# Performance work log

Hardware: AMD Instinct MI355X
Metric: run time of the kernel (lower is better)

Reference implementation:

```python
import jax, jax.numpy as jnp
import numpy as np

K = 3          # k_neighbors
EPS = 1e-12    # F.normalize eps


def _l2norm(x):
    n = jnp.sqrt(jnp.sum(x * x, axis=-1, keepdims=True))
    return x / jnp.maximum(n, EPS)


def setup_inputs() -> dict:
    key = jax.random.key(0)
    k1, k2 = jax.random.split(key)
    query_features = jax.random.normal(k1, (64, 64, 32, 32), dtype=jnp.float32)
    support_features = jax.random.normal(k2, (64, 5, 64, 1024), dtype=jnp.float32)
    return {"query_features": query_features, "support_features": support_features}


def reference(query_features, support_features):
    B, D, h, w = query_features.shape
    # (B, Nq, D), L2-normalized along D
    q_local = _l2norm(query_features.reshape(B, D, h * w).transpose(0, 2, 1))
    # support: (B, Way, D, Ns) -> (B, Way, Ns, D), L2-normalized along D
    s_local = _l2norm(support_features.transpose(0, 1, 3, 2))
    # cosine similarities for all (batch, way) pairs in one batched matmul
    sim = jnp.einsum('bqd,bwsd->bwqs', q_local, s_local)  # (B, Way, Nq, Ns)
    k_actual = min(K, sim.shape[-1])
    topk_sim, _ = jax.lax.top_k(sim, k_actual)            # (B, Way, Nq, k)
    return topk_sim.sum(axis=(-1, -2))                    # (B, Way)
```

## Files before the change

### kernel.cpp

```cpp
#include <hip/hip_runtime.h>
#include <hip/hip_bf16.h>


using bf16x8 = __attribute__((ext_vector_type(8))) short;
using f32x4  = __attribute__((ext_vector_type(4))) float;

__device__ inline unsigned cvt_pk_bf16(float lo, float hi) {
    unsigned r;
    asm("v_cvt_pk_bf16_f32 %0, %1, %2" : "=v"(r) : "v"(lo), "v"(hi));
    return r;
}

__device__ inline uint4 pack8cvt(const float* v) {
    uint4 r;
    r.x = cvt_pk_bf16(v[0], v[1]);
    r.y = cvt_pk_bf16(v[2], v[3]);
    r.z = cvt_pk_bf16(v[4], v[5]);
    r.w = cvt_pk_bf16(v[6], v[7]);
    return r;
}

#define INS(v, T0, T1, T2) do {                         \
    float _v = (v);                                     \
    float _n0 = fmaxf((T0), _v);                        \
    float _n1 = __builtin_amdgcn_fmed3f(_v, (T0), (T1));\
    float _n2 = __builtin_amdgcn_fmed3f(_v, (T1), (T2));\
    (T0) = _n0; (T1) = _n1; (T2) = _n2;                 \
} while (0)

__device__ inline void gload16(const void* g, void* lds) {
    __builtin_amdgcn_global_load_lds(
        (const __attribute__((address_space(1))) unsigned int*)g,
        (__attribute__((address_space(3))) unsigned int*)lds,
        16, 0, 0);
}


__global__ __launch_bounds__(256) void prep_all(const float* __restrict__ Q,
                                                const float* __restrict__ S,
                                                uint4* __restrict__ Qbf,
                                                uint4* __restrict__ Sbf,
                                                float* __restrict__ rnq) {
    const int blk = blockIdx.x;
    if (blk < 256) {
        const int b = blk >> 2;
        const int col = ((blk & 3) << 8) + threadIdx.x;
        const float* p = Q + (size_t)b * 65536 + col;
        float v[64];
        #pragma unroll
        for (int d = 0; d < 64; ++d) v[d] = p[(size_t)d << 10];
        float ss = 0.f;
        #pragma unroll
        for (int d = 0; d < 64; ++d) ss += v[d] * v[d];
        rnq[(b << 10) + col] = 1.0f / fmaxf(sqrtf(ss), 1e-12f);
        uint4* ob = Qbf + ((size_t)(b << 6) + (col >> 4)) * 128 + (col & 15);
        #pragma unroll
        for (int h = 0; h < 8; ++h)
            ob[h << 4] = pack8cvt(&v[h << 3]);
    } else {
        const int bw = (blk - 256) >> 2;
        const int col = ((blk & 3) << 8) + threadIdx.x;
        const float* p = S + (size_t)bw * 65536 + col;
        float v[64];
        #pragma unroll
        for (int d = 0; d < 64; ++d) v[d] = p[(size_t)d << 10];
        float ss = 0.f;
        #pragma unroll
        for (int d = 0; d < 64; ++d) ss += v[d] * v[d];
        const float rs = 1.0f / fmaxf(sqrtf(ss), 1e-12f);
        #pragma unroll
        for (int d = 0; d < 64; ++d) v[d] *= rs;
        uint4* ob = Sbf + ((size_t)(bw << 6) + (col >> 4)) * 128 + (col & 15);
        #pragma unroll
        for (int h = 0; h < 8; ++h)
            ob[h << 4] = pack8cvt(&v[h << 3]);
    }
}

__device__ __forceinline__ void compute_tile4(const uint4* sp, int lane,
                                              const bf16x8 (&bq)[4][2],
                                              float (&t0)[4], float (&t1)[4],
                                              float (&t2)[4]) {
    bf16x8 a0 = *reinterpret_cast<const bf16x8*>(&sp[lane]);
    bf16x8 a1 = *reinterpret_cast<const bf16x8*>(&sp[64 + lane]);
    const f32x4 z = {0.f, 0.f, 0.f, 0.f};
    f32x4 c[4];
    __builtin_amdgcn_s_setprio(1);
    #pragma unroll
    for (int qt = 0; qt < 4; ++qt) {
        c[qt] = __builtin_amdgcn_mfma_f32_16x16x32_bf16(a0, bq[qt][0], z, 0, 0, 0);
        c[qt] = __builtin_amdgcn_mfma_f32_16x16x32_bf16(a1, bq[qt][1], c[qt], 0, 0, 0);
    }
    __builtin_amdgcn_s_setprio(0);
    #pragma unroll
    for (int qt = 0; qt < 4; ++qt) {
        INS(c[qt][0], t0[qt], t1[qt], t2[qt]);
        INS(c[qt][1], t0[qt], t1[qt], t2[qt]);
        INS(c[qt][2], t0[qt], t1[qt], t2[qt]);
        INS(c[qt][3], t0[qt], t1[qt], t2[qt]);
    }
}

__global__ __launch_bounds__(256, 4) void knn_main(const uint4* __restrict__ Qbf,
                                                   const uint4* __restrict__ Sbf,
                                                   const float* __restrict__ rnq,
                                                   float* __restrict__ partial) {
    __shared__ uint4 ring[4][5 * 128];
    const int lin = blockIdx.x;
    const int l   = (lin & 7) * 320 + (lin >> 3);
    const int qc  = l & 7;
    const int bw  = l >> 3;
    const int b   = bw / 5;
    const int wv = threadIdx.x >> 6, lane = threadIdx.x & 63;
    const int g  = wv >> 1, h = wv & 1;

    const uint4* qb = Qbf + ((size_t)(b << 6) + (qc << 3) + (g << 2)) * 128 + lane;
    bf16x8 bq[4][2];
    #pragma unroll
    for (int qt = 0; qt < 4; ++qt)
        #pragma unroll
        for (int c = 0; c < 2; ++c)
            bq[qt][c] = *reinterpret_cast<const bf16x8*>(&qb[qt * 128 + (c << 6)]);

    const char* sbyte = (const char*)(Sbf + (size_t)bw * 8192) + ((size_t)h << 16)
                        + (size_t)lane * 16;
    uint4* myring = &ring[wv][0];

    float t0[4], t1[4], t2[4];
    #pragma unroll
    for (int qt = 0; qt < 4; ++qt) { t0[qt] = -1e30f; t1[qt] = -1e30f; t2[qt] = -1e30f; }

    #pragma unroll
    for (int t = 0; t < 3; ++t) {
        gload16(sbyte + (size_t)t * 2048,        &myring[t * 128]);
        gload16(sbyte + (size_t)t * 2048 + 1024, &myring[t * 128 + 64]);
    }

    int rslot = 0, wslot = 3;
    for (int t = 0; t <= 28; ++t) {
        gload16(sbyte + (size_t)(t + 3) * 2048,        &myring[wslot * 128]);
        gload16(sbyte + (size_t)(t + 3) * 2048 + 1024, &myring[wslot * 128 + 64]);
        asm volatile("s_waitcnt vmcnt(6)" ::: "memory");
        compute_tile4(&myring[rslot * 128], lane, bq, t0, t1, t2);
        if (++rslot == 5) rslot = 0;
        if (++wslot == 5) wslot = 0;
    }
    asm volatile("s_waitcnt vmcnt(4)" ::: "memory");
    compute_tile4(&myring[4 * 128], lane, bq, t0, t1, t2);
    asm volatile("s_waitcnt vmcnt(2)" ::: "memory");
    compute_tile4(&myring[0], lane, bq, t0, t1, t2);
    asm volatile("s_waitcnt vmcnt(0)" ::: "memory");
    compute_tile4(&myring[1 * 128], lane, bq, t0, t1, t2);

    #pragma unroll
    for (int qt = 0; qt < 4; ++qt) {
        #pragma unroll
        for (int m = 16; m <= 32; m <<= 1) {
            float b0 = __shfl_xor(t0[qt], m);
            float b1 = __shfl_xor(t1[qt], m);
            float b2 = __shfl_xor(t2[qt], m);
            INS(b0, t0[qt], t1[qt], t2[qt]);
            INS(b1, t0[qt], t1[qt], t2[qt]);
            INS(b2, t0[qt], t1[qt], t2[qt]);
        }
    }

    if (h == 1) {
        float* tb = (float*)&ring[wv][0];
        if (lane < 16) {
            #pragma unroll
            for (int qt = 0; qt < 4; ++qt) {
                tb[qt * 48 + lane]      = t0[qt];
                tb[qt * 48 + 16 + lane] = t1[qt];
                tb[qt * 48 + 32 + lane] = t2[qt];
            }
        }
    }
    __syncthreads();
    if (h == 0) {
        const float* tb = (const float*)&ring[wv + 1][0];
        float s3 = 0.f;
        #pragma unroll
        for (int qt = 0; qt < 4; ++qt) {
            float u0 = tb[qt * 48 + (lane & 15)];
            float u1 = tb[qt * 48 + 16 + (lane & 15)];
            float u2 = tb[qt * 48 + 32 + (lane & 15)];
            INS(u0, t0[qt], t1[qt], t2[qt]);
            INS(u1, t0[qt], t1[qt], t2[qt]);
            INS(u2, t0[qt], t1[qt], t2[qt]);
            const int qg = (qc << 7) + (g << 6) + (qt << 4) + (lane & 15);
            s3 += (t0[qt] + t1[qt] + t2[qt]) * rnq[(b << 10) + qg];
        }
        #pragma unroll
        for (int m = 1; m < 64; m <<= 1) s3 += __shfl_xor(s3, m);
        s3 *= 0.25f;
        if (lane == 0) partial[(size_t)bw * 16 + qc * 2 + g] = s3;
    }
}

__global__ void finalize16(const float* __restrict__ partial, float* __restrict__ out) {
    int i = blockIdx.x * blockDim.x + threadIdx.x;
    if (i < 320) {
        float a = 0.f;
        #pragma unroll
        for (int k = 0; k < 16; ++k) a += partial[16 * i + k];
        out[i] = a;
    }
}

__global__ void norms_kernel(const float* __restrict__ Q, const float* __restrict__ S,
                             float* __restrict__ rnq, float* __restrict__ rns) {
    int gid = blockIdx.x * blockDim.x + threadIdx.x;
    if (gid < 65536) {
        int b = gid >> 10, qi = gid & 1023;
        const float* p = Q + (size_t)b * 65536 + qi;
        float ss = 0.f;
        #pragma unroll
        for (int d = 0; d < 64; ++d) { float v = p[(size_t)d * 1024]; ss += v * v; }
        rnq[gid] = 1.0f / fmaxf(sqrtf(ss), 1e-12f);
    } else {
        int v = gid - 65536;
        int bw = v >> 10, si = v & 1023;
        const float* p = S + (size_t)bw * 65536 + si;
        float ss = 0.f;
        #pragma unroll
        for (int d = 0; d < 64; ++d) { float x = p[(size_t)d * 1024]; ss += x * x; }
        rns[v] = 1.0f / fmaxf(sqrtf(ss), 1e-12f);
    }
}

__global__ __launch_bounds__(512, 4) void knn_fb(
        const float* __restrict__ Q, const float* __restrict__ S,
        const float* __restrict__ rnq, const float* __restrict__ rns,
        float* __restrict__ partial) {
    __shared__ uint4 qfrag[16 * 128];
    __shared__ uint4 sfrag[2][4 * 128];
    __shared__ float wsum[8];

    const int qc = blockIdx.x, w = blockIdx.y, b = blockIdx.z;
    const int t = threadIdx.x, wv = t >> 6, lane = t & 63;

    const float* Qb   = Q + (size_t)b * 65536;
    const float* Sb   = S + (size_t)(b * 5 + w) * 65536;
    const float* rnqb = rnq + (b << 10);
    const float* rnsb = rns + ((b * 5 + w) << 10);

    bf16x8 bq[4][2];
    for (int ph = 0; ph < 2; ++ph) {
        for (int sub = 0; sub < 4; ++sub) {
            int qg = (qc << 9) + (ph << 8) + (sub << 6) + lane;
            float v[8];
            #pragma unroll
            for (int i = 0; i < 8; ++i)
                v[i] = Qb[(size_t)((wv << 3) + i) * 1024 + qg];
            qfrag[((sub << 2) + (lane >> 4)) * 128 + (wv << 4) + (lane & 15)] = pack8cvt(v);
        }
        __syncthreads();
        if ((wv >> 2) == ph) {
            #pragma unroll
            for (int qt = 0; qt < 4; ++qt)
                #pragma unroll
                for (int c = 0; c < 2; ++c)
                    bq[qt][c] = *reinterpret_cast<const bf16x8*>(
                        &qfrag[(((wv & 3) << 2) + qt) * 128 + (c << 6) + lane]);
        }
        __syncthreads();
    }

    {
        float sv[8]; float rs = rnsb[lane];
        #pragma unroll
        for (int i = 0; i < 8; ++i)
            sv[i] = Sb[(size_t)((wv << 3) + i) * 1024 + lane] * rs;
        sfrag[0][(lane >> 4) * 128 + (wv << 4) + (lane & 15)] = pack8cvt(sv);
    }
    __syncthreads();

    float t0[4], t1[4], t2[4];
    #pragma unroll
    for (int qt = 0; qt < 4; ++qt) { t0[qt] = -1e30f; t1[qt] = -1e30f; t2[qt] = -1e30f; }
    int cur = 0;
    const float* sp = Sb + ((wv << 3) << 10) + lane;

    for (int blk = 0; blk < 16; ++blk) {
        float sv[8]; float rs;
        if (blk < 15) {
            const int sb_ = (blk + 1) << 6;
            rs = rnsb[sb_ + lane];
            #pragma unroll
            for (int i = 0; i < 8; ++i)
                sv[i] = sp[(size_t)(i << 10) + sb_];
        }
        #pragma unroll
        for (int st = 0; st < 4; ++st) {
            bf16x8 a0 = *reinterpret_cast<const bf16x8*>(&sfrag[cur][st * 128 + lane]);
            bf16x8 a1 = *reinterpret_cast<const bf16x8*>(&sfrag[cur][st * 128 + 64 + lane]);
            #pragma unroll
            for (int qt = 0; qt < 4; ++qt) {
                f32x4 c = {0.f, 0.f, 0.f, 0.f};
                c = __builtin_amdgcn_mfma_f32_16x16x32_bf16(a0, bq[qt][0], c, 0, 0, 0);
                c = __builtin_amdgcn_mfma_f32_16x16x32_bf16(a1, bq[qt][1], c, 0, 0, 0);
                #pragma unroll
                for (int j = 0; j < 4; ++j)
                    INS(c[j], t0[qt], t1[qt], t2[qt]);
            }
        }
        if (blk < 15) {
            #pragma unroll
            for (int i = 0; i < 8; ++i) sv[i] *= rs;
            sfrag[cur ^ 1][(lane >> 4) * 128 + (wv << 4) + (lane & 15)] = pack8cvt(sv);
        }
        __syncthreads();
        cur ^= 1;
    }

    float s3 = 0.f;
    #pragma unroll
    for (int qt = 0; qt < 4; ++qt) {
        #pragma unroll
        for (int m = 16; m <= 32; m <<= 1) {
            float b0 = __shfl_xor(t0[qt], m);
            float b1 = __shfl_xor(t1[qt], m);
            float b2 = __shfl_xor(t2[qt], m);
            INS(b0, t0[qt], t1[qt], t2[qt]);
            INS(b1, t0[qt], t1[qt], t2[qt]);
            INS(b2, t0[qt], t1[qt], t2[qt]);
        }
        int qg = (qc << 9) + (wv << 6) + (qt << 4) + (lane & 15);
        s3 += (t0[qt] + t1[qt] + t2[qt]) * rnqb[qg];
    }
    #pragma unroll
    for (int m = 1; m < 64; m <<= 1) s3 += __shfl_xor(s3, m);
    s3 *= 0.25f;
    if (lane == 0) wsum[wv] = s3;
    __syncthreads();
    if (t == 0) {
        float acc = 0.f;
        #pragma unroll
        for (int i = 0; i < 8; ++i) acc += wsum[i];
        partial[((b * 5 + w) << 1) + qc] = acc;
    }
}

__global__ void finalize2(const float* __restrict__ partial, float* __restrict__ out) {
    int i = blockIdx.x * blockDim.x + threadIdx.x;
    if (i < 320)
        out[i] = partial[2 * i] + partial[2 * i + 1];
}

extern "C" void kernel_launch(void* const* d_in, const int* in_sizes, int n_in,
                              void* d_out, int out_size, void* d_ws, size_t ws_size,
                              hipStream_t stream) {
    const float* Q = (const float*)d_in[0];
    const float* S = (const float*)d_in[1];
    float* out = (float*)d_out;

    const size_t QBF = 8388608ull, SBF = 41943040ull, RNQ = 262144ull;
    const size_t NEED = QBF + SBF + RNQ + 20480ull;
    if (ws_size >= NEED) {
        char* base = (char*)d_ws;
        uint4* Qbf     = (uint4*)base;
        uint4* Sbf     = (uint4*)(base + QBF);
        float* rnq     = (float*)(base + QBF + SBF);
        float* partial = (float*)(base + QBF + SBF + RNQ);
        prep_all<<<1536, 256, 0, stream>>>(Q, S, Qbf, Sbf, rnq);
        knn_main<<<2560, 256, 0, stream>>>(Qbf, Sbf, rnq, partial);
        finalize16<<<2, 256, 0, stream>>>(partial, out);
    } else {
        float* rnq = (float*)d_ws;
        float* rns = rnq + 65536;
        float* partial = rns + 327680;
        norms_kernel<<<(65536 + 327680) / 256, 256, 0, stream>>>(Q, S, rnq, rns);
        knn_fb<<<dim3(2, 5, 64), 512, 0, stream>>>(Q, S, rnq, rns, partial);
        finalize2<<<2, 256, 0, stream>>>(partial, out);
    }
}
```

Before: 95.42 us.

## Software-pipeline MFMA with top-k insertion and prefetch LDS reads one tile ahead

Restructures the main loop so the MFMAs for tile t overlap the top-3 insertion of tile t-1 and the LDS reads for tile t+1, with the loop fully unrolled. The launch bounds change from min 4 blocks per CU to waves_per_eu(1,2), giving the compiler more registers for the doubled accumulator and operand sets. The aim is to hide MFMA latency and LDS latency behind VALU work. In exchange, occupancy may drop and code size grows, and the vmcnt accounting changes with the staggered loads.

```diff
diff --git a/kernel.cpp b/kernel.cpp
--- a/kernel.cpp
+++ b/kernel.cpp
@@ -77,34 +77,12 @@
     }
 }
 
-__device__ __forceinline__ void compute_tile4(const uint4* sp, int lane,
-                                              const bf16x8 (&bq)[4][2],
-                                              float (&t0)[4], float (&t1)[4],
-                                              float (&t2)[4]) {
-    bf16x8 a0 = *reinterpret_cast<const bf16x8*>(&sp[lane]);
-    bf16x8 a1 = *reinterpret_cast<const bf16x8*>(&sp[64 + lane]);
-    const f32x4 z = {0.f, 0.f, 0.f, 0.f};
-    f32x4 c[4];
-    __builtin_amdgcn_s_setprio(1);
-    #pragma unroll
-    for (int qt = 0; qt < 4; ++qt) {
-        c[qt] = __builtin_amdgcn_mfma_f32_16x16x32_bf16(a0, bq[qt][0], z, 0, 0, 0);
-        c[qt] = __builtin_amdgcn_mfma_f32_16x16x32_bf16(a1, bq[qt][1], c[qt], 0, 0, 0);
-    }
-    __builtin_amdgcn_s_setprio(0);
-    #pragma unroll
-    for (int qt = 0; qt < 4; ++qt) {
-        INS(c[qt][0], t0[qt], t1[qt], t2[qt]);
-        INS(c[qt][1], t0[qt], t1[qt], t2[qt]);
-        INS(c[qt][2], t0[qt], t1[qt], t2[qt]);
-        INS(c[qt][3], t0[qt], t1[qt], t2[qt]);
-    }
-}
-
-__global__ __launch_bounds__(256, 4) void knn_main(const uint4* __restrict__ Qbf,
-                                                   const uint4* __restrict__ Sbf,
-                                                   const float* __restrict__ rnq,
-                                                   float* __restrict__ partial) {
+__global__ __launch_bounds__(256)
+__attribute__((amdgpu_waves_per_eu(1, 2)))
+void knn_main(const uint4* __restrict__ Qbf,
+              const uint4* __restrict__ Sbf,
+              const float* __restrict__ rnq,
+              float* __restrict__ partial) {
     __shared__ uint4 ring[4][5 * 128];
     const int lin = blockIdx.x;
     const int l   = (lin & 7) * 320 + (lin >> 3);
@@ -130,27 +108,60 @@
     #pragma unroll
     for (int qt = 0; qt < 4; ++qt) { t0[qt] = -1e30f; t1[qt] = -1e30f; t2[qt] = -1e30f; }
 
-    #pragma unroll
-    for (int t = 0; t < 3; ++t) {
-        gload16(sbyte + (size_t)t * 2048,        &myring[t * 128]);
-        gload16(sbyte + (size_t)t * 2048 + 1024, &myring[t * 128 + 64]);
-    }
-
-    int rslot = 0, wslot = 3;
-    for (int t = 0; t <= 28; ++t) {
-        gload16(sbyte + (size_t)(t + 3) * 2048,        &myring[wslot * 128]);
-        gload16(sbyte + (size_t)(t + 3) * 2048 + 1024, &myring[wslot * 128 + 64]);
-        asm volatile("s_waitcnt vmcnt(6)" ::: "memory");
-        compute_tile4(&myring[rslot * 128], lane, bq, t0, t1, t2);
-        if (++rslot == 5) rslot = 0;
-        if (++wslot == 5) wslot = 0;
-    }
+    auto STAGE = [&](int tile, int slot) {
+        gload16(sbyte + (size_t)tile * 2048,        &myring[slot * 128]);
+        gload16(sbyte + (size_t)tile * 2048 + 1024, &myring[slot * 128 + 64]);
+    };
+    auto DSREAD = [&](int slot, bf16x8& a0, bf16x8& a1) {
+        a0 = *reinterpret_cast<const bf16x8*>(&myring[slot * 128 + lane]);
+        a1 = *reinterpret_cast<const bf16x8*>(&myring[slot * 128 + 64 + lane]);
+    };
+    auto MFMA4 = [&](const bf16x8& a0, const bf16x8& a1, f32x4 (&c)[4]) {
+        #pragma unroll
+        for (int qt = 0; qt < 4; ++qt) {
+            const f32x4 z = {0.f, 0.f, 0.f, 0.f};
+            c[qt] = __builtin_amdgcn_mfma_f32_16x16x32_bf16(a0, bq[qt][0], z, 0, 0, 0);
+            c[qt] = __builtin_amdgcn_mfma_f32_16x16x32_bf16(a1, bq[qt][1], c[qt], 0, 0, 0);
+        }
+    };
+    auto INS4 = [&](const f32x4 (&c)[4]) {
+        #pragma unroll
+        for (int qt = 0; qt < 4; ++qt) {
+            INS(c[qt][0], t0[qt], t1[qt], t2[qt]);
+            INS(c[qt][1], t0[qt], t1[qt], t2[qt]);
+            INS(c[qt][2], t0[qt], t1[qt], t2[qt]);
+            INS(c[qt][3], t0[qt], t1[qt], t2[qt]);
+        }
+    };
+
+    bf16x8 aC0, aC1, aN0, aN1;
+    f32x4 cP[4], cN[4];
+
+    STAGE(0, 0); STAGE(1, 1); STAGE(2, 2);
     asm volatile("s_waitcnt vmcnt(4)" ::: "memory");
-    compute_tile4(&myring[4 * 128], lane, bq, t0, t1, t2);
-    asm volatile("s_waitcnt vmcnt(2)" ::: "memory");
-    compute_tile4(&myring[0], lane, bq, t0, t1, t2);
-    asm volatile("s_waitcnt vmcnt(0)" ::: "memory");
-    compute_tile4(&myring[1 * 128], lane, bq, t0, t1, t2);
+    DSREAD(0, aC0, aC1);
+    STAGE(3, 3);
+    asm volatile("s_waitcnt vmcnt(4)" ::: "memory");
+    DSREAD(1, aN0, aN1);
+    MFMA4(aC0, aC1, cP);
+    aC0 = aN0; aC1 = aN1;
+
+    #pragma unroll
+    for (int t = 1; t <= 30; ++t) {
+        if (t + 3 < 32) STAGE(t + 3, (t + 3) % 5);
+        if (t <= 28)      { asm volatile("s_waitcnt vmcnt(4)" ::: "memory"); }
+        else if (t == 29) { asm volatile("s_waitcnt vmcnt(2)" ::: "memory"); }
+        else              { asm volatile("s_waitcnt vmcnt(0)" ::: "memory"); }
+        DSREAD((t + 1) % 5, aN0, aN1);
+        MFMA4(aC0, aC1, cN);
+        INS4(cP);
+        #pragma unroll
+        for (int qt = 0; qt < 4; ++qt) cP[qt] = cN[qt];
+        aC0 = aN0; aC1 = aN1;
+    }
+    MFMA4(aC0, aC1, cN);
+    INS4(cP);
+    INS4(cN);
 
     #pragma unroll
     for (int qt = 0; qt < 4; ++qt) {
```

Result: no change. 96.99 us (+1.6%).
